# Kernel optimization log

Measured on AMD Instinct MI355X. Metric: run time of the kernel, lower is better.

The kernel has to match this reference:

```python
import jax, jax.numpy as jnp
import numpy as np

KS = 3                 # kernel_size
DILATIONS = (1, 2, 3)  # dilation list
NUM_HEADS = 6


def _unfold_reflect(x, ks, dil):
    """ReflectionPad2d(dil*(ks-1)//2) + Unfold(ks, dilation=dil).
    x: [B, C, H, W] -> [B, C*ks*ks, H, W] (channel-major like torch Unfold)."""
    pad = dil * (ks - 1) // 2
    xp = jnp.pad(x, ((0, 0), (0, 0), (pad, pad), (pad, pad)), mode='reflect')
    return jax.lax.conv_general_dilated_patches(
        xp, filter_shape=(ks, ks), window_strides=(1, 1), padding='VALID',
        rhs_dilation=(dil, dil))  # [B, C*ks*ks, H, W]


def _dilate_attention(q, k, v, head_dim, ks, dil):
    """q,k,v: [B, c2, H, W] -> [B, H, W, c2]."""
    B, c2, H, W = q.shape
    nh = c2 // head_dim
    scale = head_dim ** (-0.5)
    P = H * W
    k2 = ks * ks
    # q -> [B, nh, P, hd]
    qr = q.reshape(B, nh, head_dim, P).transpose(0, 1, 3, 2)
    # unfold k, v -> [B, c2*k2, H, W], channel order (c, kh, kw)
    ku = _unfold_reflect(k, ks, dil).reshape(B, nh, head_dim, k2, P)
    vu = _unfold_reflect(v, ks, dil).reshape(B, nh, head_dim, k2, P)
    kr = ku.transpose(0, 1, 4, 2, 3)  # [B, nh, P, hd, k2]
    vr = vu.transpose(0, 1, 4, 3, 2)  # [B, nh, P, k2, hd]
    scores = jnp.einsum('bnpd,bnpdk->bnpk', qr, kr) * scale
    attn = jax.nn.softmax(scores, axis=-1)
    out = jnp.einsum('bnpk,bnpkd->bnpd', attn, vr)  # [B, nh, P, hd]
    return out.transpose(0, 2, 1, 3).reshape(B, H, W, nh * head_dim)


def _forward(x, pos_w, pos_b, qkv_w, proj_w):
    B, C, H, W = x.shape
    nd = len(DILATIONS)
    c2 = C // nd
    head_dim = C // NUM_HEADS
    # depthwise 3x3 positional conv (groups=C) + residual
    pe = jax.lax.conv_general_dilated(
        x, pos_w, window_strides=(1, 1), padding=((1, 1), (1, 1)),
        dimension_numbers=('NCHW', 'OIHW', 'NCHW'), feature_group_count=C)
    x = x + pe + pos_b[None, :, None, None]
    # 1x1 qkv conv
    qkv = jnp.einsum('oc,bchw->bohw', qkv_w, x)  # [B, 3C, H, W]
    # 'b (three nd c2) h w -> nd three b c2 h w'
    qkv = qkv.reshape(B, 3, nd, c2, H, W).transpose(2, 1, 0, 3, 4, 5)
    outs = []
    for i, dil in enumerate(DILATIONS):
        o = _dilate_attention(qkv[i, 0], qkv[i, 1], qkv[i, 2], head_dim, KS, dil)
        outs.append(o.transpose(0, 3, 1, 2))  # [B, c2, H, W]
    xo = jnp.concatenate(outs, axis=1)  # [B, C, H, W], dilation-major channels
    return jnp.einsum('oc,bchw->bohw', proj_w, xo)


def setup_inputs() -> dict:
    key = jax.random.key(0)
    ks = jax.random.split(key, 5)
    B, C, H, W = 4, 192, 128, 128
    return {
        'x': jax.random.normal(ks[0], (B, C, H, W), dtype=jnp.float32),
        'pos_w': jax.random.normal(ks[1], (C, 1, 3, 3), dtype=jnp.float32) * 0.05,
        'pos_b': jax.random.normal(ks[2], (C,), dtype=jnp.float32) * 0.05,
        'qkv_w': jax.random.normal(ks[3], (3 * C, C), dtype=jnp.float32) * (C ** -0.5),
        'proj_w': jax.random.normal(ks[4], (C, C), dtype=jnp.float32) * (C ** -0.5),
    }


def reference(x, pos_w, pos_b, qkv_w, proj_w):
    return _forward(x, pos_w, pos_b, qkv_w, proj_w)
```

## Files before the change

kernel.cpp:

```cpp
#include <hip/hip_runtime.h>
#include <hip/hip_bf16.h>
#include <math.h>

#define Hdim 128
#define Wdim 128
#define HW   16384
#define Cdim 192
#define Bdim 4
#define QKVC 576
#define NTOT (Bdim * HW)

typedef __attribute__((ext_vector_type(8))) short short8;
typedef __attribute__((ext_vector_type(4))) short short4v;
typedef __attribute__((ext_vector_type(4))) float f32x4;

__device__ __forceinline__ void async_ld16(void* lds, const void* g) {
    __builtin_amdgcn_global_load_lds(
        (const __attribute__((address_space(1))) void*)g,
        (__attribute__((address_space(3))) void*)lds, 16, 0, 0);
}
__device__ __forceinline__ float lo16(unsigned u) { return __uint_as_float(u << 16); }
__device__ __forceinline__ float hi16(unsigned u) { return __uint_as_float(u & 0xffff0000u); }

__global__ void convert_w(const float* __restrict__ qkv_w,
                          const float* __restrict__ proj_w,
                          __hip_bfloat16* __restrict__ Wq,
                          __hip_bfloat16* __restrict__ Wp) {
    int i = blockIdx.x * 256 + threadIdx.x;
    if (i < QKVC * Cdim) {
        Wq[i] = __float2bfloat16(qkv_w[i]);
    } else {
        int j = i - QKVC * Cdim;
        Wp[j] = __float2bfloat16(proj_w[j]);
    }
}

__global__ __launch_bounds__(256, 5)
void posconv_nhwc(const float* __restrict__ x,
                  const float* __restrict__ pos_w,
                  const float* __restrict__ pos_b,
                  __hip_bfloat16* __restrict__ Xb) {
    __shared__ __align__(16) float xs[3 * 16 * 128];
    __shared__ __hip_bfloat16 tile[16][132];

    int t = threadIdx.x;
    int id = blockIdx.x;
    int xj = id & 7;
    int r_ = id >> 3;
    int rb = r_ & 15;
    int cg = (r_ >> 4) % 12;
    int b  = (r_ >> 4) / 12;
    int h  = xj * 16 + rb;

    int hh0 = h > 0 ? h - 1 : 0;
    int hh1 = h;
    int hh2 = h < Hdim - 1 ? h + 1 : Hdim - 1;

    int ch = t >> 4;
    int qh = t & 15;
    int cglob = cg * 16 + ch;

    const float* wp = pos_w + cglob * 9;
    float w0 = wp[0], w1 = wp[1], w2 = wp[2];
    float w3 = wp[3], w4 = wp[4], w5 = wp[5];
    float w6 = wp[6], w7 = wp[7], w8 = wp[8];
    float bias = pos_b[cglob];
    float m0 = (h > 0) ? 1.f : 0.f;
    float m2 = (h < Hdim - 1) ? 1.f : 0.f;
    w0 *= m0; w1 *= m0; w2 *= m0;
    w6 *= m2; w7 *= m2; w8 *= m2;

    {
        const float* xg = x + (size_t)(b * Cdim + cg * 16) * HW;
#pragma unroll
        for (int k = 0; k < 6; ++k) {
            int u = t + k * 256;
            int rowi = u >> 5;
            int ql = u & 31;
            int rr = rowi >> 4;
            int sch = rowi & 15;
            int hr = rr == 0 ? hh0 : (rr == 1 ? hh1 : hh2);
            int qs = ql ^ sch;
            async_ld16((char*)xs + (size_t)u * 16,
                       xg + (size_t)sch * HW + hr * Wdim + qs * 4);
        }
    }
    __syncthreads();

    float out[8];
    {
        const char* xsb = (const char*)xs;
        const char* r0b = xsb + (size_t)(0 * 16 + ch) * 512;
        const char* r1b = xsb + (size_t)(1 * 16 + ch) * 512;
        const char* r2b = xsb + (size_t)(2 * 16 + ch) * 512;
        float4 lo0 = *(const float4*)(r0b + (((2 * qh)     ^ ch) * 16));
        float4 hi0 = *(const float4*)(r0b + (((2 * qh + 1) ^ ch) * 16));
        float4 lo1 = *(const float4*)(r1b + (((2 * qh)     ^ ch) * 16));
        float4 hi1 = *(const float4*)(r1b + (((2 * qh + 1) ^ ch) * 16));
        float4 lo2 = *(const float4*)(r2b + (((2 * qh)     ^ ch) * 16));
        float4 hi2 = *(const float4*)(r2b + (((2 * qh + 1) ^ ch) * 16));
        float L0 = __shfl_up(hi0.w, 1, 64), R0 = __shfl_down(lo0.x, 1, 64);
        float L1 = __shfl_up(hi1.w, 1, 64), R1 = __shfl_down(lo1.x, 1, 64);
        float L2 = __shfl_up(hi2.w, 1, 64), R2 = __shfl_down(lo2.x, 1, 64);
        if (qh == 0)  { L0 = 0.f; L1 = 0.f; L2 = 0.f; }
        if (qh == 15) { R0 = 0.f; R1 = 0.f; R2 = 0.f; }
        float a0[10] = {L0, lo0.x, lo0.y, lo0.z, lo0.w, hi0.x, hi0.y, hi0.z, hi0.w, R0};
        float a1[10] = {L1, lo1.x, lo1.y, lo1.z, lo1.w, hi1.x, hi1.y, hi1.z, hi1.w, R1};
        float a2[10] = {L2, lo2.x, lo2.y, lo2.z, lo2.w, hi2.x, hi2.y, hi2.z, hi2.w, R2};
#pragma unroll
        for (int i = 0; i < 8; ++i) {
            out[i] = a1[i + 1] + bias
                   + w0 * a0[i] + w1 * a0[i + 1] + w2 * a0[i + 2]
                   + w3 * a1[i] + w4 * a1[i + 1] + w5 * a1[i + 2]
                   + w6 * a2[i] + w7 * a2[i + 1] + w8 * a2[i + 2];
        }
    }

    union { unsigned short u[8]; short8 v; } pk;
#pragma unroll
    for (int i = 0; i < 8; ++i) {
        __hip_bfloat16 bv = __float2bfloat16(out[i]);
        pk.u[i] = *(unsigned short*)&bv;
    }
    *(short8*)(void*)&tile[ch][qh * 8] = pk.v;
    __syncthreads();

    int px = t >> 1, s2 = t & 1;
    union { unsigned short u[8]; short8 v; } o;
#pragma unroll
    for (int j = 0; j < 8; ++j)
        o.u[j] = *(const unsigned short*)&tile[s2 * 8 + j][px];
    size_t p0img = (size_t)(b << 14) + (size_t)h * Wdim;
    *(short8*)(void*)(Xb + (p0img + px) * Cdim + cg * 16 + s2 * 8) = o.v;
}

template <int MODE, int MT>
__global__ __launch_bounds__(256, 3)
void gemm_mfma(const __hip_bfloat16* __restrict__ Wb,
               const __hip_bfloat16* __restrict__ Xt,
               void* __restrict__ Cout) {
    __shared__ __hip_bfloat16 As[2][64 * 32];
    __shared__ __hip_bfloat16 Bs[2][256 * 32];
    const int t = threadIdx.x;
    const int w = t >> 6, l = t & 63;
    const int lq = l >> 4, lr = l & 15;
    const int id = blockIdx.x;
    const int xj = id & 7;
    const int rest = id >> 3;
    const int m0 = (rest % MT) * 64;
    const int n0 = ((rest / MT) * 8 + xj) * 256;

    const int ms = t >> 2, kcs = t & 3;

    auto stage = [&](int buf, int kt_) {
        const int k0_ = kt_ * 32;
        async_ld16(As[buf] + t * 8,
                   Wb + (size_t)(m0 + ms) * Cdim + k0_ + kcs * 8);
#pragma unroll
        for (int it = 0; it < 4; ++it) {
            int idx = it * 256 + t;
            int n = idx >> 2, kc = idx & 3;
            const __hip_bfloat16* src;
            if (MODE == 0)
                src = Xt + (size_t)(n0 + n) * Cdim + k0_ + kc * 8;
            else
                src = Xt + (size_t)kt_ * ((size_t)NTOT * 32) +
                      (size_t)(n0 + n) * 32 + kc * 8;
            async_ld16(Bs[buf] + idx * 8, src);
        }
    };

    f32x4 acc[4][4] = {};

    stage(0, 0);
    __syncthreads();

#pragma unroll
    for (int kt = 0; kt < 6; ++kt) {
        const int cur = kt & 1;
        if (kt < 5) stage(cur ^ 1, kt + 1);

        short8 af[4], bf[4];
#pragma unroll
        for (int i = 0; i < 4; ++i)
            af[i] = *(const short8*)(void*)(As[cur] + (i * 16 + lr) * 32 + lq * 8);
#pragma unroll
        for (int j = 0; j < 4; ++j)
            bf[j] = *(const short8*)(void*)(Bs[cur] + (w * 64 + j * 16 + lr) * 32 + lq * 8);
#pragma unroll
        for (int i = 0; i < 4; ++i)
#pragma unroll
            for (int j = 0; j < 4; ++j)
                acc[i][j] = __builtin_amdgcn_mfma_f32_16x16x32_bf16(
                    af[i], bf[j], acc[i][j], 0, 0, 0);

        __syncthreads();
    }

#pragma unroll
    for (int i = 0; i < 4; ++i) {
        int mb = m0 + i * 16 + lq * 4;
#pragma unroll
        for (int j = 0; j < 4; ++j) {
            int n = n0 + w * 64 + j * 16 + lr;
            if (MODE == 0) {
                int three = mb / 192, rem = mb % 192;
                int pi = rem >> 6, pn = (rem >> 5) & 1, d4 = rem & 31;
                size_t plane = (size_t)((three * 3 + pi) * 2 + pn);
                __hip_bfloat16* dst = (__hip_bfloat16*)Cout +
                    plane * ((size_t)NTOT * 32) + (size_t)n * 32 + d4;
                short4v pk;
#pragma unroll
                for (int r = 0; r < 4; ++r) {
                    __hip_bfloat16 bv = __float2bfloat16(acc[i][j][r]);
                    pk[r] = *(short*)&bv;
                }
                *(short4v*)(void*)dst = pk;
            } else {
                int b = n >> 14, p = n & (HW - 1);
#pragma unroll
                for (int r = 0; r < 4; ++r)
                    ((float*)Cout)[((size_t)(b * Cdim + mb + r)) * HW + p] =
                        acc[i][j][r];
            }
        }
    }
}

__global__ __launch_bounds__(512, 2)
void attn_proj(const __hip_bfloat16* __restrict__ QKV,
               const __hip_bfloat16* __restrict__ Wpg,
               float* __restrict__ out) {
    __shared__ __align__(16) unsigned char smem[151552];
    unsigned char* kv  = smem;
    unsigned char* aob = smem + 98304;
    unsigned char* wpl = smem;

    const int t = threadIdx.x;
    const int px = t >> 2, s = t & 3;
    const int id = blockIdx.x;
    const int xj = id & 7, rest = id >> 3;
    const int b = rest >> 4, rb = rest & 15;
    const int h = xj * 16 + rb;
    const size_t PS = (size_t)NTOT * 32;
    const size_t colbase = (size_t)(b << 14) + (size_t)h * Wdim;

    uint4 qv[6];
#pragma unroll
    for (int c = 0; c < 6; ++c)
        qv[c] = *((const uint4*)(QKV + (size_t)c * PS + (colbase + px) * 32) + s);

    const int g = t ^ ((t >> 3) & 7);

    auto stageKV = [&](int buf, int comb) {
        int dil = (comb >> 1) + 1;
        unsigned char* base = kv + buf * 49152;
#pragma unroll
        for (int kh = 0; kh < 3; ++kh) {
            int v = h + (kh - 1) * dil;
            v = v < 0 ? -v : (v >= Hdim ? 2 * Hdim - 2 - v : v);
            size_t rowe = ((size_t)(b << 14) + (size_t)v * Wdim) * 32;
            async_ld16(base + (kh * 512 + t) * 16,
                       QKV + (size_t)(6 + comb) * PS + rowe + g * 8);
            async_ld16(base + ((kh + 3) * 512 + t) * 16,
                       QKV + (size_t)(12 + comb) * PS + rowe + g * 8);
        }
    };

    stageKV(0, 0);
    __syncthreads();

#pragma unroll
    for (int c = 0; c < 6; ++c) {
        if (c < 5) stageKV((c + 1) & 1, c + 1);

        {
            const int dil = (c >> 1) + 1;
            const unsigned char* base = kv + (c & 1) * 49152;
            float q[8];
            {
                uint4 x = qv[c];
                q[0] = lo16(x.x); q[1] = hi16(x.x);
                q[2] = lo16(x.y); q[3] = hi16(x.y);
                q[4] = lo16(x.z); q[5] = hi16(x.z);
                q[6] = lo16(x.w); q[7] = hi16(x.w);
            }
            int coff[3];
#pragma unroll
            for (int kw = 0; kw < 3; ++kw) {
                int ww = px + (kw - 1) * dil;
                ww = ww < 0 ? -ww : (ww >= Wdim ? 2 * Wdim - 2 - ww : ww);
                int i0 = 4 * ww + s;
                coff[kw] = (i0 ^ ((i0 >> 3) & 7)) * 16;
            }
            float sc[9];
#pragma unroll
            for (int kh = 0; kh < 3; ++kh)
#pragma unroll
                for (int kw = 0; kw < 3; ++kw) {
                    uint4 xk = *(const uint4*)(void*)(base + kh * 8192 + coff[kw]);
                    sc[kh * 3 + kw] =
                          q[0] * lo16(xk.x) + q[1] * hi16(xk.x)
                        + q[2] * lo16(xk.y) + q[3] * hi16(xk.y)
                        + q[4] * lo16(xk.z) + q[5] * hi16(xk.z)
                        + q[6] * lo16(xk.w) + q[7] * hi16(xk.w);
                }
#pragma unroll
            for (int j = 0; j < 9; ++j) {
                float v = sc[j];
                v += __shfl_xor(v, 1, 64);
                v += __shfl_xor(v, 2, 64);
                sc[j] = v * 0.17677669529663687f;
            }
            float mx = sc[0];
#pragma unroll
            for (int j = 1; j < 9; ++j) mx = fmaxf(mx, sc[j]);
            float sum = 0.f;
#pragma unroll
            for (int j = 0; j < 9; ++j) { sc[j] = __expf(sc[j] - mx); sum += sc[j]; }
            float inv = 1.f / sum;

            float a8[8] = {};
#pragma unroll
            for (int kh = 0; kh < 3; ++kh)
#pragma unroll
                for (int kw = 0; kw < 3; ++kw) {
                    float a = sc[kh * 3 + kw];
                    uint4 xv = *(const uint4*)(void*)(base + (kh + 3) * 8192 + coff[kw]);
                    a8[0] += a * lo16(xv.x); a8[1] += a * hi16(xv.x);
                    a8[2] += a * lo16(xv.y); a8[3] += a * hi16(xv.y);
                    a8[4] += a * lo16(xv.z); a8[5] += a * hi16(xv.z);
                    a8[6] += a * lo16(xv.w); a8[7] += a * hi16(xv.w);
                }
            union { unsigned short u[8]; short8 v; } pk;
#pragma unroll
            for (int d2 = 0; d2 < 8; ++d2) {
                __hip_bfloat16 bv = __float2bfloat16(a8[d2] * inv);
                pk.u[d2] = *(unsigned short*)&bv;
            }
            *(short8*)(void*)(aob + px * 416 + c * 64 + s * 16) = pk.v;
        }
        __syncthreads();
    }

#pragma unroll
    for (int k = 0; k < 10; ++k) {
        if (k < 9 || t < 384) {
            int cidx = t + k * 512;
            int row = cidx / 26, c16 = cidx % 26;
            async_ld16(wpl + (size_t)cidx * 16, Wpg + row * 192 + c16 * 8);
        }
    }
    __syncthreads();

    const int wv = t >> 6, l = t & 63;
    const int lq = l >> 4, lr = l & 15;
    f32x4 pacc[12] = {};
#pragma unroll
    for (int kt = 0; kt < 6; ++kt) {
        short8 bfrag = *(const short8*)(void*)
            (aob + (wv * 16 + lr) * 416 + kt * 64 + lq * 16);
#pragma unroll
        for (int i = 0; i < 12; ++i) {
            short8 afrag = *(const short8*)(void*)
                (wpl + (i * 16 + lr) * 416 + kt * 64 + lq * 16);
            pacc[i] = __builtin_amdgcn_mfma_f32_16x16x32_bf16(
                afrag, bfrag, pacc[i], 0, 0, 0);
        }
    }
    float* outp = out + (size_t)b * Cdim * HW + (size_t)h * Wdim;
#pragma unroll
    for (int i = 0; i < 12; ++i) {
        int o = i * 16 + lq * 4;
        int pxn = wv * 16 + lr;
#pragma unroll
        for (int r = 0; r < 4; ++r)
            outp[(size_t)(o + r) * HW + pxn] = pacc[i][r];
    }
}

extern "C" void kernel_launch(void* const* d_in, const int* in_sizes, int n_in,
                              void* d_out, int out_size, void* d_ws, size_t ws_size,
                              hipStream_t stream) {
    const float* x      = (const float*)d_in[0];
    const float* pos_w  = (const float*)d_in[1];
    const float* pos_b  = (const float*)d_in[2];
    const float* qkv_w  = (const float*)d_in[3];
    const float* proj_w = (const float*)d_in[4];
    float* out = (float*)d_out;

    char* ws = (char*)d_ws;
    __hip_bfloat16* Xb  = (__hip_bfloat16*)ws;
    __hip_bfloat16* QKV = (__hip_bfloat16*)(ws + (size_t)25165824);
    __hip_bfloat16* Wq  = (__hip_bfloat16*)(ws + (size_t)125829120);
    __hip_bfloat16* Wp  = (__hip_bfloat16*)(ws + (size_t)126050304);

    convert_w<<<(QKVC * Cdim + Cdim * Cdim) / 256, 256, 0, stream>>>(
        qkv_w, proj_w, Wq, Wp);

    posconv_nhwc<<<6144, 256, 0, stream>>>(x, pos_w, pos_b, Xb);

    gemm_mfma<0, 9><<<2304, 256, 0, stream>>>(Wq, Xb, QKV);

    attn_proj<<<512, 512, 0, stream>>>(QKV, Wp, out);
}
```

Before: 178.9 us.

## Shrink attn_proj LDS by single-buffering KV and keeping attention output in registers

Cuts the attn_proj shared-memory footprint from about 148KB to 75KB so four 512-thread blocks can be resident instead of two. The KV double buffer becomes a single buffer, so each dilation's stage now waits behind a barrier instead of overlapping with compute. The attention output buffer is removed: per-pixel results stay in registers and are redistributed to MFMA B fragments with cross-lane shuffles. The projection weight tile padding also shrinks from 26 to 25 16-byte chunks per row. In exchange it loses load/compute overlap and raises register pressure under a tighter launch bound.

Result: slower. 260.5 us (+45.6%).

```diff
diff --git a/kernel.cpp b/kernel.cpp
--- a/kernel.cpp
+++ b/kernel.cpp
@@ -227,13 +227,12 @@
     }
 }
 
-__global__ __launch_bounds__(512, 2)
+__global__ __launch_bounds__(512, 4)
 void attn_proj(const __hip_bfloat16* __restrict__ QKV,
                const __hip_bfloat16* __restrict__ Wpg,
                float* __restrict__ out) {
-    __shared__ __align__(16) unsigned char smem[151552];
+    __shared__ __align__(16) unsigned char smem[76800];
     unsigned char* kv  = smem;
-    unsigned char* aob = smem + 98304;
     unsigned char* wpl = smem;
 
     const int t = threadIdx.x;
@@ -252,31 +251,29 @@
 
     const int g = t ^ ((t >> 3) & 7);
 
-    auto stageKV = [&](int buf, int comb) {
+    auto stageKV = [&](int comb) {
         int dil = (comb >> 1) + 1;
-        unsigned char* base = kv + buf * 49152;
 #pragma unroll
         for (int kh = 0; kh < 3; ++kh) {
             int v = h + (kh - 1) * dil;
             v = v < 0 ? -v : (v >= Hdim ? 2 * Hdim - 2 - v : v);
             size_t rowe = ((size_t)(b << 14) + (size_t)v * Wdim) * 32;
-            async_ld16(base + (kh * 512 + t) * 16,
+            async_ld16(kv + (kh * 512 + t) * 16,
                        QKV + (size_t)(6 + comb) * PS + rowe + g * 8);
-            async_ld16(base + ((kh + 3) * 512 + t) * 16,
+            async_ld16(kv + ((kh + 3) * 512 + t) * 16,
                        QKV + (size_t)(12 + comb) * PS + rowe + g * 8);
         }
     };
 
-    stageKV(0, 0);
+    unsigned pa[6][4];
+
+    stageKV(0);
     __syncthreads();
 
 #pragma unroll
     for (int c = 0; c < 6; ++c) {
-        if (c < 5) stageKV((c + 1) & 1, c + 1);
-
         {
             const int dil = (c >> 1) + 1;
-            const unsigned char* base = kv + (c & 1) * 49152;
             float q[8];
             {
                 uint4 x = qv[c];
@@ -298,7 +295,7 @@
             for (int kh = 0; kh < 3; ++kh)
 #pragma unroll
                 for (int kw = 0; kw < 3; ++kw) {
-                    uint4 xk = *(const uint4*)(void*)(base + kh * 8192 + coff[kw]);
+                    uint4 xk = *(const uint4*)(void*)(kv + kh * 8192 + coff[kw]);
                     sc[kh * 3 + kw] =
                           q[0] * lo16(xk.x) + q[1] * hi16(xk.x)
                         + q[2] * lo16(xk.y) + q[3] * hi16(xk.y)
@@ -326,44 +323,52 @@
 #pragma unroll
                 for (int kw = 0; kw < 3; ++kw) {
                     float a = sc[kh * 3 + kw];
-                    uint4 xv = *(const uint4*)(void*)(base + (kh + 3) * 8192 + coff[kw]);
+                    uint4 xv = *(const uint4*)(void*)(kv + (kh + 3) * 8192 + coff[kw]);
                     a8[0] += a * lo16(xv.x); a8[1] += a * hi16(xv.x);
                     a8[2] += a * lo16(xv.y); a8[3] += a * hi16(xv.y);
                     a8[4] += a * lo16(xv.z); a8[5] += a * hi16(xv.z);
                     a8[6] += a * lo16(xv.w); a8[7] += a * hi16(xv.w);
                 }
-            union { unsigned short u[8]; short8 v; } pk;
-#pragma unroll
-            for (int d2 = 0; d2 < 8; ++d2) {
-                __hip_bfloat16 bv = __float2bfloat16(a8[d2] * inv);
-                pk.u[d2] = *(unsigned short*)&bv;
+#pragma unroll
+            for (int j = 0; j < 4; ++j) {
+                __hip_bfloat16 blo = __float2bfloat16(a8[2 * j]     * inv);
+                __hip_bfloat16 bhi = __float2bfloat16(a8[2 * j + 1] * inv);
+                pa[c][j] = (unsigned)*(unsigned short*)&blo |
+                           ((unsigned)*(unsigned short*)&bhi << 16);
             }
-            *(short8*)(void*)(aob + px * 416 + c * 64 + s * 16) = pk.v;
         }
         __syncthreads();
+        if (c < 5) {
+            stageKV(c + 1);
+            __syncthreads();
+        }
     }
 
 #pragma unroll
     for (int k = 0; k < 10; ++k) {
-        if (k < 9 || t < 384) {
+        if (k < 9 || t < 192) {
             int cidx = t + k * 512;
-            int row = cidx / 26, c16 = cidx % 26;
-            async_ld16(wpl + (size_t)cidx * 16, Wpg + row * 192 + c16 * 8);
+            int row = cidx / 25, cc = cidx - row * 25;
+            async_ld16(wpl + (size_t)cidx * 16, Wpg + row * 192 + cc * 8);
         }
     }
     __syncthreads();
 
     const int wv = t >> 6, l = t & 63;
     const int lq = l >> 4, lr = l & 15;
+    const int srcl = (l & 15) * 4 + (l >> 4);
     f32x4 pacc[12] = {};
 #pragma unroll
     for (int kt = 0; kt < 6; ++kt) {
-        short8 bfrag = *(const short8*)(void*)
-            (aob + (wv * 16 + lr) * 416 + kt * 64 + lq * 16);
+        union { unsigned d[4]; short8 v; } bu;
+#pragma unroll
+        for (int j = 0; j < 4; ++j)
+            bu.d[j] = (unsigned)__shfl((int)pa[kt][j], srcl, 64);
+        short8 bfrag = bu.v;
 #pragma unroll
         for (int i = 0; i < 12; ++i) {
             short8 afrag = *(const short8*)(void*)
-                (wpl + (i * 16 + lr) * 416 + kt * 64 + lq * 16);
+                (wpl + (size_t)((i * 16 + lr) * 25 + kt * 4 + lq) * 16);
             pacc[i] = __builtin_amdgcn_mfma_f32_16x16x32_bf16(
                 afrag, bfrag, pacc[i], 0, 0, 0);
         }
```
